# Kernel tuning notes

Hardware: AMD Instinct MI355X
Metric: run time of the kernel (lower is better)

Reference implementation:

```python
import jax, jax.numpy as jnp
import numpy as np

D_MODEL = 1024
N_HEADS = 16
D_K = D_MODEL // N_HEADS
THETA = 10000.0
BATCH = 1
SEQ = 4096


def setup_inputs() -> dict:
    key = jax.random.key(0)
    ks = jax.random.split(key, 5)
    std = (2.0 / (D_MODEL + D_MODEL)) ** 0.5
    mk = lambda k: jax.random.truncated_normal(k, -3.0, 3.0, (D_MODEL, D_MODEL), jnp.float32) * std
    return {
        "x": jax.random.normal(ks[0], (BATCH, SEQ, D_MODEL), jnp.float32),
        "Wq": mk(ks[1]),
        "Wk": mk(ks[2]),
        "Wv": mk(ks[3]),
        "Wo": mk(ks[4]),
    }


def _rope(x, pos, inv_freq):
    # x: [b, h, s, d_k]; pos: [s]; inv_freq: [d_k/2]
    angles = pos[:, None].astype(jnp.float32) * inv_freq  # [s, d_k/2]
    cos = jnp.repeat(jnp.cos(angles), 2, axis=-1)  # [s, d_k]
    sin = jnp.repeat(jnp.sin(angles), 2, axis=-1)
    # interleaved rotation: (-x1, x0, -x3, x2, ...)
    x_rot = jnp.stack([-x[..., 1::2], x[..., 0::2]], axis=-1).reshape(x.shape)
    return x * cos + x_rot * sin


def reference(x, Wq, Wk, Wv, Wo):
    b, s, _ = x.shape
    h, dk = N_HEADS, D_K
    proj = lambda W: jnp.einsum('bsi,oi->bso', x, W).reshape(b, s, h, dk).transpose(0, 2, 1, 3)
    q = proj(Wq)
    k = proj(Wk)
    v = proj(Wv)
    pos = jnp.arange(s)
    inv_freq = 1.0 / THETA ** (jnp.arange(0, dk, 2, dtype=jnp.float32) / dk)
    q = _rope(q, pos, inv_freq)
    k = _rope(k, pos, inv_freq)
    scores = jnp.einsum('bhqd,bhkd->bhqk', q, k) / jnp.sqrt(jnp.asarray(dk, jnp.float32))
    causal_mask = jnp.arange(s)[None, :] > jnp.arange(s)[:, None]  # [s, s], True above diag
    scores = jnp.where(causal_mask, -jnp.inf, scores)
    weights = jax.nn.softmax(scores, axis=-1)
    out = jnp.einsum('bhqk,bhkd->bhqd', weights, v)
    out = out.transpose(0, 2, 1, 3).reshape(b, s, h * dk)
    return jnp.einsum('bsi,oi->bso', out, Wo)
```

## Files before the change

kernel.cpp:

```cpp
#include <hip/hip_runtime.h>
#include <hip/hip_bf16.h>


typedef __hip_bfloat16 bf16;
using s16x4 = __attribute__((ext_vector_type(4))) short;
using s16x8 = __attribute__((ext_vector_type(8))) short;
using f32x4 = __attribute__((ext_vector_type(4))) float;

#define SEQ 4096
#define DMODEL 1024
#define NHEADS 16
#define DK 64
#define LOG2_THETA 13.287712379549449f
#define SCALE_LOG2E 0.1803368801111244f

#if defined(__has_builtin)
#if __has_builtin(__builtin_amdgcn_mfma_f32_16x16x16bf16_1k)
#define HAVE_MFMA16 1
#endif
#endif

__device__ __forceinline__ f32x4 mfma16(s16x4 a, s16x4 b, f32x4 c) {
#ifdef HAVE_MFMA16
  return __builtin_amdgcn_mfma_f32_16x16x16bf16_1k(a, b, c, 0, 0, 0);
#else
  asm volatile("v_mfma_f32_16x16x16_bf16 %0, %1, %2, %0"
               : "+v"(c) : "v"(a), "v"(b));
  return c;
#endif
}

__device__ __forceinline__ void async16(const bf16* g, bf16* l) {
  __builtin_amdgcn_global_load_lds(
      (const __attribute__((address_space(1))) unsigned int*)g,
      (__attribute__((address_space(3))) unsigned int*)l, 16, 0, 0);
}

__global__ __launch_bounds__(256)
void conv_kernel(const float* __restrict__ s0, const float* __restrict__ s1,
                 const float* __restrict__ s2, const float* __restrict__ s3,
                 const float* __restrict__ s4,
                 bf16* __restrict__ d0, bf16* __restrict__ d1,
                 bf16* __restrict__ d2, bf16* __restrict__ d3,
                 bf16* __restrict__ d4) {
  const int z = blockIdx.z;
  const float* s = (z == 0) ? s0 : (z == 1) ? s1 : (z == 2) ? s2 : (z == 3) ? s3 : s4;
  bf16* d = (z == 0) ? d0 : (z == 1) ? d1 : (z == 2) ? d2 : (z == 3) ? d3 : d4;
  const int n = (z == 0) ? SEQ * DMODEL : DMODEL * DMODEL;
  const int i = (blockIdx.x * 256 + threadIdx.x) * 8;
  if (i >= n) return;
  const float4 a = *(const float4*)(s + i);
  const float4 b = *(const float4*)(s + i + 4);
  union { bf16 h[8]; s16x8 v; } u;
  u.h[0] = __float2bfloat16(a.x); u.h[1] = __float2bfloat16(a.y);
  u.h[2] = __float2bfloat16(a.z); u.h[3] = __float2bfloat16(a.w);
  u.h[4] = __float2bfloat16(b.x); u.h[5] = __float2bfloat16(b.y);
  u.h[6] = __float2bfloat16(b.z); u.h[7] = __float2bfloat16(b.w);
  *(s16x8*)(d + i) = u.v;
}

__global__ __launch_bounds__(256)
void gemm_kernel(const bf16* __restrict__ A,
                 const bf16* __restrict__ W0, const bf16* __restrict__ W1,
                 const bf16* __restrict__ W2,
                 bf16* __restrict__ D0, bf16* __restrict__ D1,
                 bf16* __restrict__ D2, float* __restrict__ Df,
                 int mode_base) {
  const int mode = mode_base + (int)blockIdx.z;
  const bf16* __restrict__ W = (mode == 1) ? W1 : (mode == 2) ? W2 : W0;
  bf16* __restrict__ D = (mode == 1) ? D1 : (mode == 2) ? D2 : D0;

  const int tid  = threadIdx.x;
  const int lane = tid & 63;
  const int wave = tid >> 6;
  const int wm = wave >> 1, wn = wave & 1;
  const int quad = lane >> 4, l16 = lane & 15;
  const int m0 = blockIdx.x * 128;
  const int n0 = blockIdx.y * 128;

  __shared__ __align__(16) bf16 As[128 * 32];
  __shared__ __align__(16) bf16 Bs[128 * 32];
  __shared__ __align__(16) bf16 Es[4][64 * 64];

  f32x4 acc[4][4] = {};

  const int ldrow = lane >> 2;
  const int ldcol = (lane & 3) * 8;

  for (int k0 = 0; k0 < DMODEL; k0 += 32) {
#pragma unroll
    for (int c = 0; c < 2; ++c) {
      const int chunk = wave * 2 + c;
      const int row = chunk * 16 + ldrow;
      async16(&A[(size_t)(m0 + row) * DMODEL + k0 + ldcol], &As[chunk * 512]);
      async16(&W[(size_t)(n0 + row) * DMODEL + k0 + ldcol], &Bs[chunk * 512]);
    }
    __syncthreads();

    s16x8 af[4], bfr[4];
#pragma unroll
    for (int i = 0; i < 4; ++i)
      af[i] = *(const s16x8*)&As[(wm * 64 + i * 16 + l16) * 32 + quad * 8];
#pragma unroll
    for (int j = 0; j < 4; ++j)
      bfr[j] = *(const s16x8*)&Bs[(wn * 64 + j * 16 + l16) * 32 + quad * 8];
#pragma unroll
    for (int i = 0; i < 4; ++i)
#pragma unroll
      for (int j = 0; j < 4; ++j)
        acc[i][j] = __builtin_amdgcn_mfma_f32_16x16x32_bf16(af[i], bfr[j],
                                                            acc[i][j], 0, 0, 0);
    __syncthreads();
  }

  if (mode == 3) {
#pragma unroll
    for (int i = 0; i < 4; ++i)
#pragma unroll
      for (int j = 0; j < 4; ++j) {
        const int col = n0 + wn * 64 + j * 16 + l16;
#pragma unroll
        for (int r = 0; r < 4; ++r) {
          const int srow = m0 + wm * 64 + i * 16 + quad * 4 + r;
          Df[(size_t)srow * DMODEL + col] = acc[i][j][r];
        }
      }
    return;
  }

  if (mode == 2) {
#pragma unroll
    for (int i = 0; i < 4; ++i)
#pragma unroll
      for (int j = 0; j < 4; ++j)
#pragma unroll
        for (int r = 0; r < 4; ++r)
          Es[wave][(j * 16 + l16) * 64 + i * 16 + quad * 4 + r] =
              __float2bfloat16(acc[i][j][r]);
  } else {
#pragma unroll
    for (int i = 0; i < 4; ++i)
#pragma unroll
      for (int j = 0; j < 4; ++j)
#pragma unroll
        for (int r = 0; r < 4; ++r)
          Es[wave][(i * 16 + quad * 4 + r) * 64 + j * 16 + l16] =
              __float2bfloat16(acc[i][j][r]);
  }
  __syncthreads();

  const int h = (n0 >> 6) + wn;
  const int g  = lane >> 3;
  const int c8 = (lane & 7) * 8;

  if (mode == 2) {
#pragma unroll
    for (int t = 0; t < 8; ++t) {
      const int d = t * 8 + g;
      const s16x8 v = *(const s16x8*)&Es[wave][d * 64 + c8];
      *(s16x8*)&D[((size_t)h * DK + d) * SEQ + m0 + wm * 64 + c8] = v;
    }
  } else {
    const float qs = (mode == 0) ? SCALE_LOG2E : 1.0f;
    float sn[4], cs[4], s8[4], c8r[4], invf[4];
    const int srow0 = m0 + wm * 64 + g;
#pragma unroll
    for (int k = 0; k < 4; ++k) {
      const int p = (c8 >> 1) + k;
      invf[k] = __builtin_amdgcn_exp2f((float)p * (-2.0f / 64.0f) * LOG2_THETA);
      sincosf((float)srow0 * invf[k], &sn[k], &cs[k]);
      sincosf(8.0f * invf[k], &s8[k], &c8r[k]);
      sn[k] *= qs; cs[k] *= qs;
    }
#pragma unroll
    for (int t = 0; t < 8; ++t) {
      const int rl = t * 8 + g;
      union { bf16 h[8]; s16x8 v; } u, o;
      u.v = *(const s16x8*)&Es[wave][rl * 64 + c8];
#pragma unroll
      for (int k = 0; k < 4; ++k) {
        const float x0 = __bfloat162float(u.h[2 * k]);
        const float x1 = __bfloat162float(u.h[2 * k + 1]);
        o.h[2 * k]     = __float2bfloat16(x0 * cs[k] - x1 * sn[k]);
        o.h[2 * k + 1] = __float2bfloat16(x1 * cs[k] + x0 * sn[k]);
        const float ns_ = sn[k] * c8r[k] + cs[k] * s8[k];
        cs[k] = cs[k] * c8r[k] - sn[k] * s8[k];
        sn[k] = ns_;
      }
      const int srow = m0 + wm * 64 + rl;
      *(s16x8*)&D[((size_t)h * SEQ + srow) * DK + c8] = o.v;
    }
  }
}

__global__ __launch_bounds__(256, 4)
void attn_kernel(const bf16* __restrict__ Q, const bf16* __restrict__ K,
                 const bf16* __restrict__ Vt, bf16* __restrict__ O) {
  const int tid  = threadIdx.x;
  const int lane = tid & 63;
  const int wave = tid >> 6;
  const int quad = lane >> 4, l16 = lane & 15;
  const int wq = wave & 1;
  const int wk = wave >> 1;

  const int i  = (int)blockIdx.x;
  const int j  = i & 255;
  const int vv = 3 - (i >> 8);
  const int h  = j & 15;
  const int a  = j >> 4;
  const int qb = vv * 16 + ((vv & 1) ? (15 - a) : a);

  const bf16* __restrict__ Qh = Q + (size_t)h * SEQ * DK;
  const bf16* __restrict__ Kh = K + (size_t)h * SEQ * DK;
  const bf16* __restrict__ Vh = Vt + (size_t)h * DK * SEQ;

  __shared__ __align__(16) char smemb[32768];
  bf16* __restrict__ smem = (bf16*)smemb;
  bf16* __restrict__ KsB = smem;
  bf16* __restrict__ VsB = smem + 8192;

  const int srow = lane >> 3;
  const int schk = (lane & 7) ^ srow;
  const int xsw  = l16 & 7;

  const int q0 = qb * 64;
  const int qw = q0 + wq * 32;
  const int nb = qb + 1;

  s16x8 aq[2][2];
#pragma unroll
  for (int gq = 0; gq < 2; ++gq) {
    const size_t qr = (size_t)(qw + gq * 16 + l16) * DK;
    aq[gq][0] = *(const s16x8*)&Qh[qr + quad * 8];
    aq[gq][1] = *(const s16x8*)&Qh[qr + 32 + quad * 8];
  }

  f32x4 oacc[2][4] = {};
  float lsum[2] = {0.f, 0.f};

  {
#pragma unroll
    for (int c = 0; c < 2; ++c) {
      const int chunk = wave * 2 + c;
      async16(Kh + (size_t)(chunk * 8 + srow) * 64 + schk * 8,
              &KsB[chunk * 512]);
      async16(Vh + (size_t)(chunk * 8 + srow) * SEQ + schk * 8,
              &VsB[chunk * 512]);
    }
  }
  __syncthreads();

  for (int kb = 0; kb < nb; ++kb) {
    const int cur = kb & 1;
    if (kb + 1 < nb) {
      const int nxt = cur ^ 1;
      const int kv1 = (kb + 1) * 64;
      const bf16* kg = Kh + (size_t)kv1 * DK;
#pragma unroll
      for (int c = 0; c < 2; ++c) {
        const int chunk = wave * 2 + c;
        async16(kg + (size_t)(chunk * 8 + srow) * 64 + schk * 8,
                &KsB[nxt * 4096 + chunk * 512]);
        async16(Vh + (size_t)(chunk * 8 + srow) * SEQ + kv1 + schk * 8,
                &VsB[nxt * 4096 + chunk * 512]);
      }
    }

    const bf16* __restrict__ Ksc = &KsB[cur * 4096];
    const bf16* __restrict__ Vsc = &VsB[cur * 4096];

    f32x4 sc[2][2] = {};
    __builtin_amdgcn_s_setprio(1);
#pragma unroll
    for (int hh = 0; hh < 2; ++hh) {
      const bf16* kr = &Ksc[(wk * 32 + hh * 16 + l16) * 64];
      const s16x8 ak0 = *(const s16x8*)&kr[(quad ^ xsw) * 8];
      const s16x8 ak1 = *(const s16x8*)&kr[((quad + 4) ^ xsw) * 8];
#pragma unroll
      for (int gq = 0; gq < 2; ++gq) {
        sc[gq][hh] = __builtin_amdgcn_mfma_f32_16x16x32_bf16(ak0, aq[gq][0], sc[gq][hh], 0, 0, 0);
        sc[gq][hh] = __builtin_amdgcn_mfma_f32_16x16x32_bf16(ak1, aq[gq][1], sc[gq][hh], 0, 0, 0);
      }
    }
    __builtin_amdgcn_s_setprio(0);

    if (kb == nb - 1) {
#pragma unroll
      for (int gq = 0; gq < 2; ++gq) {
        const int lim = wq * 32 + gq * 16 + l16 - wk * 32 - quad * 4;
#pragma unroll
        for (int hh = 0; hh < 2; ++hh)
#pragma unroll
          for (int r = 0; r < 4; ++r)
            if (hh * 16 + r > lim) sc[gq][hh][r] = -1e30f;
      }
    }

    s16x4 ap[2][2];
#pragma unroll
    for (int gq = 0; gq < 2; ++gq) {
#pragma unroll
      for (int hh = 0; hh < 2; ++hh) {
        union { bf16 b[4]; s16x4 v; } pk;
        float ps = 0.f;
#pragma unroll
        for (int r = 0; r < 4; ++r) {
          const float p = __builtin_amdgcn_exp2f(sc[gq][hh][r]);
          pk.b[r] = __float2bfloat16(p);
          ps += p;
        }
        lsum[gq] += ps;
        ap[gq][hh] = pk.v;
      }
    }

    __builtin_amdgcn_s_setprio(1);
#pragma unroll
    for (int hh = 0; hh < 2; ++hh) {
      const int cg = wk * 4 + hh * 2 + (quad >> 1);
      const int eo = ((cg ^ xsw) << 3) + (quad & 1) * 4;
#pragma unroll
      for (int ns = 0; ns < 4; ++ns) {
        const s16x4 bv = *(const s16x4*)&Vsc[(ns * 16 + l16) * 64 + eo];
#pragma unroll
        for (int gq = 0; gq < 2; ++gq)
          oacc[gq][ns] = mfma16(ap[gq][hh], bv, oacc[gq][ns]);
      }
    }
    __builtin_amdgcn_s_setprio(0);

    __syncthreads();
  }

  float* __restrict__ Ored = (float*)smemb;
  float* __restrict__ lred = (float*)(smemb + 16896);
  bf16*  __restrict__ Obuf = (bf16*)(smemb + 17408);

#pragma unroll
  for (int gq = 0; gq < 2; ++gq) {
    lsum[gq] += __shfl_xor(lsum[gq], 16);
    lsum[gq] += __shfl_xor(lsum[gq], 32);
  }

  if (wk == 0) {
    if (quad == 0)
#pragma unroll
      for (int gq = 0; gq < 2; ++gq)
        lred[wq * 32 + gq * 16 + l16] = lsum[gq];
  } else {
#pragma unroll
    for (int gq = 0; gq < 2; ++gq)
#pragma unroll
      for (int ns = 0; ns < 4; ++ns)
#pragma unroll
        for (int r = 0; r < 4; ++r)
          Ored[(wq * 32 + gq * 16 + quad * 4 + r) * 66 + ns * 16 + l16] =
              oacc[gq][ns][r];
  }
  __syncthreads();
  if (wk == 1 && quad == 0) {
#pragma unroll
    for (int gq = 0; gq < 2; ++gq)
      lred[wq * 32 + gq * 16 + l16] += lsum[gq];
  }
  __syncthreads();
  if (wk == 0) {
#pragma unroll
    for (int gq = 0; gq < 2; ++gq) {
      float rl[4];
#pragma unroll
      for (int r = 0; r < 4; ++r)
        rl[r] = __builtin_amdgcn_rcpf(lred[wq * 32 + gq * 16 + quad * 4 + r]);
#pragma unroll
      for (int ns = 0; ns < 4; ++ns)
#pragma unroll
        for (int r = 0; r < 4; ++r) {
          const int row = wq * 32 + gq * 16 + quad * 4 + r;
          const float v = oacc[gq][ns][r] + Ored[row * 66 + ns * 16 + l16];
          Obuf[row * 72 + ns * 16 + l16] = __float2bfloat16(v * rl[r]);
        }
    }
  }
  __syncthreads();
#pragma unroll
  for (int p = 0; p < 2; ++p) {
    const int row = p * 32 + (tid >> 3);
    const int c8 = (tid & 7) * 8;
    const s16x8 v = *(const s16x8*)&Obuf[row * 72 + c8];
    *(s16x8*)&O[(size_t)(q0 + row) * DMODEL + h * DK + c8] = v;
  }
}

extern "C" void kernel_launch(void* const* d_in, const int* in_sizes, int n_in,
                              void* d_out, int out_size, void* d_ws, size_t ws_size,
                              hipStream_t stream) {
  const float* x  = (const float*)d_in[0];
  const float* Wq = (const float*)d_in[1];
  const float* Wk = (const float*)d_in[2];
  const float* Wv = (const float*)d_in[3];
  const float* Wo = (const float*)d_in[4];
  float* out = (float*)d_out;

  bf16* ws = (bf16*)d_ws;
  bf16* xb   = ws;
  bf16* Wqb  = xb  + (size_t)SEQ * DMODEL;
  bf16* Wkb  = Wqb + (size_t)DMODEL * DMODEL;
  bf16* Wvb  = Wkb + (size_t)DMODEL * DMODEL;
  bf16* Wob  = Wvb + (size_t)DMODEL * DMODEL;
  bf16* Qb   = Wob + (size_t)DMODEL * DMODEL;
  bf16* Kb   = Qb  + (size_t)SEQ * DMODEL;
  bf16* Vtb  = Kb  + (size_t)SEQ * DMODEL;
  bf16* Attn = Vtb + (size_t)SEQ * DMODEL;

  conv_kernel<<<dim3(SEQ * DMODEL / (256 * 8), 1, 5), 256, 0, stream>>>(
      x, Wq, Wk, Wv, Wo, xb, Wqb, Wkb, Wvb, Wob);
  gemm_kernel<<<dim3(SEQ / 128, DMODEL / 128, 3), 256, 0, stream>>>(
      xb, Wqb, Wkb, Wvb, Qb, Kb, Vtb, out, 0);
  attn_kernel<<<dim3(64 * NHEADS), 256, 0, stream>>>(Qb, Kb, Vtb, Attn);
  gemm_kernel<<<dim3(SEQ / 128, DMODEL / 128, 1), 256, 0, stream>>>(
      Attn, Wob, Wob, Wob, Attn, Attn, Attn, out, 3);
}
```

Baseline: 208.1 us.

## Double-buffer GEMM loads, split output GEMM, MFMA row sums, grid-stride conversion

The QKV GEMM now double-buffers its LDS tiles so the async global-to-LDS load of the next K slice is issued before the current slice's MFMAs, with one barrier per step. The output projection moves to its own kernel with 64-row tiles, which doubles its block count to fill more CUs. The attention softmax row sum is computed by an MFMA against a ones vector instead of scalar adds and cross-lane shuffles. The conversion kernel becomes a grid-stride loop over a fixed 512-block grid. The prefetch is issued after the previous barrier without a wait for its completion before the next compute step, so it depends on the final barrier covering the outstanding async loads. Larger LDS use may also lower occupancy.

Result: faster. 187.1 us (-10.1%).

```diff
diff --git a/kernel.cpp b/kernel.cpp
--- a/kernel.cpp
+++ b/kernel.cpp
@@ -47,16 +47,16 @@
   const float* s = (z == 0) ? s0 : (z == 1) ? s1 : (z == 2) ? s2 : (z == 3) ? s3 : s4;
   bf16* d = (z == 0) ? d0 : (z == 1) ? d1 : (z == 2) ? d2 : (z == 3) ? d3 : d4;
   const int n = (z == 0) ? SEQ * DMODEL : DMODEL * DMODEL;
-  const int i = (blockIdx.x * 256 + threadIdx.x) * 8;
-  if (i >= n) return;
-  const float4 a = *(const float4*)(s + i);
-  const float4 b = *(const float4*)(s + i + 4);
-  union { bf16 h[8]; s16x8 v; } u;
-  u.h[0] = __float2bfloat16(a.x); u.h[1] = __float2bfloat16(a.y);
-  u.h[2] = __float2bfloat16(a.z); u.h[3] = __float2bfloat16(a.w);
-  u.h[4] = __float2bfloat16(b.x); u.h[5] = __float2bfloat16(b.y);
-  u.h[6] = __float2bfloat16(b.z); u.h[7] = __float2bfloat16(b.w);
-  *(s16x8*)(d + i) = u.v;
+  for (int i = (blockIdx.x * 256 + threadIdx.x) * 8; i < n; i += 512 * 256 * 8) {
+    const float4 a = *(const float4*)(s + i);
+    const float4 b = *(const float4*)(s + i + 4);
+    union { bf16 h[8]; s16x8 v; } u;
+    u.h[0] = __float2bfloat16(a.x); u.h[1] = __float2bfloat16(a.y);
+    u.h[2] = __float2bfloat16(a.z); u.h[3] = __float2bfloat16(a.w);
+    u.h[4] = __float2bfloat16(b.x); u.h[5] = __float2bfloat16(b.y);
+    u.h[6] = __float2bfloat16(b.z); u.h[7] = __float2bfloat16(b.w);
+    *(s16x8*)(d + i) = u.v;
+  }
 }
 
 __global__ __launch_bounds__(256)
@@ -64,9 +64,8 @@
                  const bf16* __restrict__ W0, const bf16* __restrict__ W1,
                  const bf16* __restrict__ W2,
                  bf16* __restrict__ D0, bf16* __restrict__ D1,
-                 bf16* __restrict__ D2, float* __restrict__ Df,
-                 int mode_base) {
-  const int mode = mode_base + (int)blockIdx.z;
+                 bf16* __restrict__ D2) {
+  const int mode = (int)blockIdx.z;
   const bf16* __restrict__ W = (mode == 1) ? W1 : (mode == 2) ? W2 : W0;
   bf16* __restrict__ D = (mode == 1) ? D1 : (mode == 2) ? D2 : D0;
 
@@ -78,32 +77,40 @@
   const int m0 = blockIdx.x * 128;
   const int n0 = blockIdx.y * 128;
 
-  __shared__ __align__(16) bf16 As[128 * 32];
-  __shared__ __align__(16) bf16 Bs[128 * 32];
-  __shared__ __align__(16) bf16 Es[4][64 * 64];
+  __shared__ __align__(16) char gsm[49152];
+  bf16* const smem = (bf16*)gsm;
 
   f32x4 acc[4][4] = {};
 
   const int ldrow = lane >> 2;
   const int ldcol = (lane & 3) * 8;
 
-  for (int k0 = 0; k0 < DMODEL; k0 += 32) {
+  auto stage = [&](int b, int k0) {
 #pragma unroll
     for (int c = 0; c < 2; ++c) {
       const int chunk = wave * 2 + c;
       const int row = chunk * 16 + ldrow;
-      async16(&A[(size_t)(m0 + row) * DMODEL + k0 + ldcol], &As[chunk * 512]);
-      async16(&W[(size_t)(n0 + row) * DMODEL + k0 + ldcol], &Bs[chunk * 512]);
-    }
-    __syncthreads();
+      async16(&A[(size_t)(m0 + row) * DMODEL + k0 + ldcol],
+              &smem[b * 8192 + chunk * 512]);
+      async16(&W[(size_t)(n0 + row) * DMODEL + k0 + ldcol],
+              &smem[b * 8192 + 4096 + chunk * 512]);
+    }
+  };
+
+  stage(0, 0);
+  __syncthreads();
+
+  for (int t = 0; t < 32; ++t) {
+    const int cur = t & 1;
+    if (t < 31) stage(cur ^ 1, (t + 1) * 32);
 
     s16x8 af[4], bfr[4];
 #pragma unroll
     for (int i = 0; i < 4; ++i)
-      af[i] = *(const s16x8*)&As[(wm * 64 + i * 16 + l16) * 32 + quad * 8];
+      af[i] = *(const s16x8*)&smem[cur * 8192 + (wm * 64 + i * 16 + l16) * 32 + quad * 8];
 #pragma unroll
     for (int j = 0; j < 4; ++j)
-      bfr[j] = *(const s16x8*)&Bs[(wn * 64 + j * 16 + l16) * 32 + quad * 8];
+      bfr[j] = *(const s16x8*)&smem[cur * 8192 + 4096 + (wn * 64 + j * 16 + l16) * 32 + quad * 8];
 #pragma unroll
     for (int i = 0; i < 4; ++i)
 #pragma unroll
@@ -113,29 +120,16 @@
     __syncthreads();
   }
 
-  if (mode == 3) {
+  bf16* const Esw = (bf16*)(gsm + 16384) + wave * 4096;
+
+  if (mode == 2) {
 #pragma unroll
     for (int i = 0; i < 4; ++i)
 #pragma unroll
-      for (int j = 0; j < 4; ++j) {
-        const int col = n0 + wn * 64 + j * 16 + l16;
-#pragma unroll
-        for (int r = 0; r < 4; ++r) {
-          const int srow = m0 + wm * 64 + i * 16 + quad * 4 + r;
-          Df[(size_t)srow * DMODEL + col] = acc[i][j][r];
-        }
-      }
-    return;
-  }
-
-  if (mode == 2) {
-#pragma unroll
-    for (int i = 0; i < 4; ++i)
-#pragma unroll
       for (int j = 0; j < 4; ++j)
 #pragma unroll
         for (int r = 0; r < 4; ++r)
-          Es[wave][(j * 16 + l16) * 64 + i * 16 + quad * 4 + r] =
+          Esw[(j * 16 + l16) * 64 + i * 16 + quad * 4 + r] =
               __float2bfloat16(acc[i][j][r]);
   } else {
 #pragma unroll
@@ -144,7 +138,7 @@
       for (int j = 0; j < 4; ++j)
 #pragma unroll
         for (int r = 0; r < 4; ++r)
-          Es[wave][(i * 16 + quad * 4 + r) * 64 + j * 16 + l16] =
+          Esw[(i * 16 + quad * 4 + r) * 64 + j * 16 + l16] =
               __float2bfloat16(acc[i][j][r]);
   }
   __syncthreads();
@@ -157,7 +151,7 @@
 #pragma unroll
     for (int t = 0; t < 8; ++t) {
       const int d = t * 8 + g;
-      const s16x8 v = *(const s16x8*)&Es[wave][d * 64 + c8];
+      const s16x8 v = *(const s16x8*)&Esw[d * 64 + c8];
       *(s16x8*)&D[((size_t)h * DK + d) * SEQ + m0 + wm * 64 + c8] = v;
     }
   } else {
@@ -176,7 +170,7 @@
     for (int t = 0; t < 8; ++t) {
       const int rl = t * 8 + g;
       union { bf16 h[8]; s16x8 v; } u, o;
-      u.v = *(const s16x8*)&Es[wave][rl * 64 + c8];
+      u.v = *(const s16x8*)&Esw[rl * 64 + c8];
 #pragma unroll
       for (int k = 0; k < 4; ++k) {
         const float x0 = __bfloat162float(u.h[2 * k]);
@@ -191,6 +185,72 @@
       *(s16x8*)&D[((size_t)h * SEQ + srow) * DK + c8] = o.v;
     }
   }
+}
+
+__global__ __launch_bounds__(256)
+void gemmo_kernel(const bf16* __restrict__ A, const bf16* __restrict__ W,
+                  float* __restrict__ Df) {
+  const int tid  = threadIdx.x;
+  const int lane = tid & 63;
+  const int wave = tid >> 6;
+  const int wm = wave >> 1, wn = wave & 1;
+  const int quad = lane >> 4, l16 = lane & 15;
+  const int m0 = blockIdx.x * 64;
+  const int n0 = blockIdx.y * 128;
+
+  __shared__ __align__(16) bf16 sm[2][6144];
+
+  f32x4 acc[2][4] = {};
+  const int ldrow = lane >> 2;
+  const int ldcol = (lane & 3) * 8;
+
+  auto stage = [&](int b, int k0) {
+    {
+      const int row = wave * 16 + ldrow;
+      async16(&A[(size_t)(m0 + row) * DMODEL + k0 + ldcol], &sm[b][wave * 512]);
+    }
+#pragma unroll
+    for (int c = 0; c < 2; ++c) {
+      const int row = (wave * 2 + c) * 16 + ldrow;
+      async16(&W[(size_t)(n0 + row) * DMODEL + k0 + ldcol],
+              &sm[b][2048 + (wave * 2 + c) * 512]);
+    }
+  };
+
+  stage(0, 0);
+  __syncthreads();
+
+  for (int t = 0; t < 32; ++t) {
+    const int cur = t & 1;
+    if (t < 31) stage(cur ^ 1, (t + 1) * 32);
+
+    s16x8 af[2], bfr[4];
+#pragma unroll
+    for (int i = 0; i < 2; ++i)
+      af[i] = *(const s16x8*)&sm[cur][(wm * 32 + i * 16 + l16) * 32 + quad * 8];
+#pragma unroll
+    for (int j = 0; j < 4; ++j)
+      bfr[j] = *(const s16x8*)&sm[cur][2048 + (wn * 64 + j * 16 + l16) * 32 + quad * 8];
+#pragma unroll
+    for (int i = 0; i < 2; ++i)
+#pragma unroll
+      for (int j = 0; j < 4; ++j)
+        acc[i][j] = __builtin_amdgcn_mfma_f32_16x16x32_bf16(af[i], bfr[j],
+                                                            acc[i][j], 0, 0, 0);
+    __syncthreads();
+  }
+
+#pragma unroll
+  for (int i = 0; i < 2; ++i)
+#pragma unroll
+    for (int j = 0; j < 4; ++j) {
+      const int col = n0 + wn * 64 + j * 16 + l16;
+#pragma unroll
+      for (int r = 0; r < 4; ++r) {
+        const int srow = m0 + wm * 32 + i * 16 + quad * 4 + r;
+        Df[(size_t)srow * DMODEL + col] = acc[i][j][r];
+      }
+    }
 }
 
 __global__ __launch_bounds__(256, 4)
@@ -227,6 +287,9 @@
   const int qw = q0 + wq * 32;
   const int nb = qb + 1;
 
+  const short ONE = 0x3F80;
+  const s16x4 ones4 = {ONE, ONE, ONE, ONE};
+
   s16x8 aq[2][2];
 #pragma unroll
   for (int gq = 0; gq < 2; ++gq) {
@@ -236,7 +299,7 @@
   }
 
   f32x4 oacc[2][4] = {};
-  float lsum[2] = {0.f, 0.f};
+  f32x4 lacc[2] = {};
 
   {
 #pragma unroll
@@ -298,21 +361,15 @@
 
     s16x4 ap[2][2];
 #pragma unroll
-    for (int gq = 0; gq < 2; ++gq) {
+    for (int gq = 0; gq < 2; ++gq)
 #pragma unroll
       for (int hh = 0; hh < 2; ++hh) {
         union { bf16 b[4]; s16x4 v; } pk;
-        float ps = 0.f;
-#pragma unroll
-        for (int r = 0; r < 4; ++r) {
-          const float p = __builtin_amdgcn_exp2f(sc[gq][hh][r]);
-          pk.b[r] = __float2bfloat16(p);
-          ps += p;
-        }
-        lsum[gq] += ps;
+#pragma unroll
+        for (int r = 0; r < 4; ++r)
+          pk.b[r] = __float2bfloat16(__builtin_amdgcn_exp2f(sc[gq][hh][r]));
         ap[gq][hh] = pk.v;
       }
-    }
 
     __builtin_amdgcn_s_setprio(1);
 #pragma unroll
@@ -327,6 +384,11 @@
           oacc[gq][ns] = mfma16(ap[gq][hh], bv, oacc[gq][ns]);
       }
     }
+#pragma unroll
+    for (int gq = 0; gq < 2; ++gq)
+#pragma unroll
+      for (int hh = 0; hh < 2; ++hh)
+        lacc[gq] = mfma16(ap[gq][hh], ones4, lacc[gq]);
     __builtin_amdgcn_s_setprio(0);
 
     __syncthreads();
@@ -336,17 +398,13 @@
   float* __restrict__ lred = (float*)(smemb + 16896);
   bf16*  __restrict__ Obuf = (bf16*)(smemb + 17408);
 
-#pragma unroll
-  for (int gq = 0; gq < 2; ++gq) {
-    lsum[gq] += __shfl_xor(lsum[gq], 16);
-    lsum[gq] += __shfl_xor(lsum[gq], 32);
-  }
-
   if (wk == 0) {
-    if (quad == 0)
+    if (l16 == 0)
 #pragma unroll
       for (int gq = 0; gq < 2; ++gq)
-        lred[wq * 32 + gq * 16 + l16] = lsum[gq];
+#pragma unroll
+        for (int r = 0; r < 4; ++r)
+          lred[wq * 32 + gq * 16 + quad * 4 + r] = lacc[gq][r];
   } else {
 #pragma unroll
     for (int gq = 0; gq < 2; ++gq)
@@ -358,10 +416,12 @@
               oacc[gq][ns][r];
   }
   __syncthreads();
-  if (wk == 1 && quad == 0) {
+  if (wk == 1 && l16 == 0) {
 #pragma unroll
     for (int gq = 0; gq < 2; ++gq)
-      lred[wq * 32 + gq * 16 + l16] += lsum[gq];
+#pragma unroll
+      for (int r = 0; r < 4; ++r)
+        lred[wq * 32 + gq * 16 + quad * 4 + r] += lacc[gq][r];
   }
   __syncthreads();
   if (wk == 0) {
@@ -412,11 +472,11 @@
   bf16* Vtb  = Kb  + (size_t)SEQ * DMODEL;
   bf16* Attn = Vtb + (size_t)SEQ * DMODEL;
 
-  conv_kernel<<<dim3(SEQ * DMODEL / (256 * 8), 1, 5), 256, 0, stream>>>(
+  conv_kernel<<<dim3(512, 1, 5), 256, 0, stream>>>(
       x, Wq, Wk, Wv, Wo, xb, Wqb, Wkb, Wvb, Wob);
   gemm_kernel<<<dim3(SEQ / 128, DMODEL / 128, 3), 256, 0, stream>>>(
-      xb, Wqb, Wkb, Wvb, Qb, Kb, Vtb, out, 0);
+      xb, Wqb, Wkb, Wvb, Qb, Kb, Vtb);
   attn_kernel<<<dim3(64 * NHEADS), 256, 0, stream>>>(Qb, Kb, Vtb, Attn);
-  gemm_kernel<<<dim3(SEQ / 128, DMODEL / 128, 1), 256, 0, stream>>>(
-      Attn, Wob, Wob, Wob, Attn, Attn, Attn, out, 3);
-}
+  gemmo_kernel<<<dim3(SEQ / 64, DMODEL / 128), 256, 0, stream>>>(
+      Attn, Wob, out);
+}
```
